# Kernel optimization log

Measured on AMD Instinct MI355X. Metric: run time of the kernel, lower is better.

## Reference

```python
import jax, jax.numpy as jnp
import numpy as np

H = 2048        # hidden size
NK = 16         # key heads
NV = 32         # value heads
DK = 128        # key head dim
DV = 128        # value head dim
K = 4           # conv kernel size
KEY_DIM = NK * DK      # 2048
VAL_DIM = NV * DV      # 4096
CONV_DIM = 2 * KEY_DIM + VAL_DIM  # 8192 (q,k,v pass through the causal conv)
EPS = 1e-6


def setup_inputs() -> dict:
    key = jax.random.key(0)
    ks = jax.random.split(key, 16)
    d = {}
    d["hidden_states"] = jax.random.normal(ks[0], (1, 1, H), jnp.float32)
    for i in range(4):
        d[f"gated_state_{i}"] = 0.1 * jax.random.normal(ks[1 + i], (1, NV, DV, DK), jnp.float32)
        d[f"conv_state_{i}"] = 0.1 * jax.random.normal(ks[5 + i], (1, K - 1, CONV_DIM), jnp.float32)
    # stacked per-layer parameters (leading dim = 4 layers)
    d["W_qkvz"] = 0.02 * jax.random.normal(ks[9], (4, H, 2 * KEY_DIM + 2 * VAL_DIM), jnp.float32)
    d["W_ba"] = 0.02 * jax.random.normal(ks[10], (4, H, 2 * NV), jnp.float32)
    d["conv_w"] = 0.1 * jax.random.normal(ks[11], (4, CONV_DIM, K), jnp.float32)
    d["dt_bias"] = 0.1 * jax.random.normal(ks[12], (4, NV), jnp.float32)
    d["A_log"] = 0.1 * jax.random.normal(ks[13], (4, NV), jnp.float32)
    d["norm_w"] = jnp.ones((4, DV), jnp.float32)
    d["W_out"] = 0.02 * jax.random.normal(ks[14], (4, VAL_DIM, H), jnp.float32)
    return d


def _layer_step(x, S, C, Wq, Wba, cw, dtb, Alog, nw, Wo):
    """One GatedDeltaNet decode step. x:[1,1,H], S:[1,NV,DV,DK], C:[1,K-1,CONV_DIM]."""
    h = x[0, 0]                                  # [H]
    qkvz = h @ Wq                                # [2*KEY + 2*VAL]
    q, k, v, z = jnp.split(qkvz, [KEY_DIM, 2 * KEY_DIM, 2 * KEY_DIM + VAL_DIM])
    ba = h @ Wba
    b, a = ba[:NV], ba[NV:]

    # causal depthwise conv state update + silu
    mixed = jnp.concatenate([q, k, v])           # [CONV_DIM]
    window = jnp.concatenate([C[0], mixed[None]], axis=0)  # [K, CONV_DIM]
    new_C = window[1:][None]                     # [1, K-1, CONV_DIM]
    conv = jax.nn.silu(jnp.einsum('kc,ck->c', window, cw))

    q, k, v = jnp.split(conv, [KEY_DIM, 2 * KEY_DIM])
    q = q.reshape(NK, DK)
    k = k.reshape(NK, DK)
    v = v.reshape(NV, DV)
    # per-head l2 norm on q, k
    q = q * jax.lax.rsqrt(jnp.sum(q * q, -1, keepdims=True) + EPS)
    k = k * jax.lax.rsqrt(jnp.sum(k * k, -1, keepdims=True) + EPS)
    rep = NV // NK
    q = jnp.repeat(q, rep, axis=0)               # [NV, DK]
    k = jnp.repeat(k, rep, axis=0)

    beta = jax.nn.sigmoid(b)                     # [NV]
    g = -jnp.exp(Alog) * jax.nn.softplus(a + dtb)
    decay = jnp.exp(g)                           # [NV]

    # gated delta-rule state update
    S0 = S[0] * decay[:, None, None]             # [NV, DV, DK]
    kv = jnp.einsum('hvd,hd->hv', S0, k)         # [NV, DV]
    S1 = S0 + jnp.einsum('hv,hd->hvd', (v - kv) * beta[:, None], k)
    o = jnp.einsum('hvd,hd->hv', S1, q) * (DK ** -0.5)  # [NV, DV]

    # gated RMSNorm over DV, gated by silu(z)
    zr = z.reshape(NV, DV)
    o = o * jax.lax.rsqrt(jnp.mean(o * o, -1, keepdims=True) + EPS) * nw
    o = o * jax.nn.silu(zr)

    y = (o.reshape(-1) @ Wo)[None, None]         # [1,1,H]
    return y, S1[None], new_C


def _forward(hidden_states, gated_states, conv_states, W_qkvz, W_ba, conv_w, dt_bias, A_log, norm_w, W_out):
    def step(x, inp):
        S, C, Wq, Wba, cw, dtb, Al, nw, Wo = inp
        y, nS, nC = _layer_step(x, S, C, Wq, Wba, cw, dtb, Al, nw, Wo)
        return y, (nS, nC)

    xf, (nS, nC) = jax.lax.scan(
        step, hidden_states,
        (gated_states, conv_states, W_qkvz, W_ba, conv_w, dt_bias, A_log, norm_w, W_out))
    return xf, nS, nC


def reference(hidden_states, gated_state_0, conv_state_0, gated_state_1, conv_state_1,
              gated_state_2, conv_state_2, gated_state_3, conv_state_3,
              W_qkvz, W_ba, conv_w, dt_bias, A_log, norm_w, W_out):
    Ss = jnp.stack([gated_state_0, gated_state_1, gated_state_2, gated_state_3])
    Cs = jnp.stack([conv_state_0, conv_state_1, conv_state_2, conv_state_3])
    xf, nS, nC = _forward(hidden_states, Ss, Cs, W_qkvz, W_ba, conv_w, dt_bias, A_log, norm_w, W_out)
    return (xf, nS[0], nC[0], nS[1], nC[1], nS[2], nC[2], nS[3], nC[3])
```

## Files before the change

kernel.cpp:

```cpp
#include <hip/hip_runtime.h>

#define H_DIM 2048
#define NV 32
#define DK 128
#define DV 128
#define KEY_DIM 2048
#define VAL_DIM 4096
#define CONV_DIM 8192
#define QKVZ_DIM 12288
#define NS_ELEMS (NV * DV * DK)
#define NC_ELEMS (3 * CONV_DIM)
#define NPQ 16
#define NPY 32

typedef float f32x4 __attribute__((ext_vector_type(4)));

__device__ __forceinline__ float silu_f(float x) { return x / (1.f + expf(-x)); }
__device__ __forceinline__ f32x4 ntload4(const float* p) {
  return __builtin_nontemporal_load(reinterpret_cast<const f32x4*>(p));
}

__global__ __launch_bounds__(256) void k_gemv_qkvz(
    const float* __restrict__ hsrc, int hparts,
    const float* __restrict__ Wq, const float* __restrict__ Wba,
    float* __restrict__ qpart, float* __restrict__ bapart)
{
  int bid = blockIdx.x, t = threadIdx.x;
  __shared__ float hs[128];
  __shared__ f32x4 red[256];
  int rb = (bid < 768) ? (bid / 48) * 128 : (bid - 768) * 128;
  if (t < 128) {
    float s = 0.f;
    if (hparts == 1) {
      s = hsrc[rb + t];
    } else {
#pragma unroll
      for (int p = 0; p < NPY; ++p) s += hsrc[p * H_DIM + rb + t];
    }
    hs[t] = s;
  }
  __syncthreads();
  if (bid < 768) {
    int p = bid / 48;
    int cb = (bid % 48) * 256;
    int jj = cb + (t & 63) * 4;
    int i0 = (t >> 6) * 32;
    f32x4 acc = {0.f, 0.f, 0.f, 0.f};
    const float* wp = Wq + (size_t)(rb + i0) * QKVZ_DIM + jj;
#pragma unroll 8
    for (int ii = 0; ii < 32; ++ii) {
      float hv = hs[i0 + ii];
      f32x4 w = ntload4(wp + (size_t)ii * QKVZ_DIM);
      acc += hv * w;
    }
    red[t] = acc;
    __syncthreads();
    if (t < 64) {
      f32x4 o = red[t] + red[t + 64] + red[t + 128] + red[t + 192];
      *reinterpret_cast<f32x4*>(qpart + (size_t)p * QKVZ_DIM + cb + t * 4) = o;
    }
  } else {
    int p = bid - 768;
    int col = t & 63;
    int i0 = (t >> 6) * 32;
    float acc = 0.f;
#pragma unroll 8
    for (int ii = 0; ii < 32; ++ii)
      acc += hs[i0 + ii] * Wba[(size_t)(rb + i0 + ii) * 64 + col];
    red[t].x = acc;
    __syncthreads();
    if (t < 64)
      bapart[p * 64 + t] = red[t].x + red[t + 64].x + red[t + 128].x + red[t + 192].x;
  }
}

__global__ __launch_bounds__(256) void k_state(
    const float* __restrict__ S_in, const float* __restrict__ C_in,
    const float* __restrict__ qpart, const float* __restrict__ bapart,
    const float* __restrict__ conv_w, const float* __restrict__ dt_bias,
    const float* __restrict__ A_log,
    float* __restrict__ nS, float* __restrict__ nC,
    float* __restrict__ o_raw, float* __restrict__ o2part)
{
  int bid = blockIdx.x, t = threadIdx.x;
  if (bid < 128) {
    int hh = bid >> 2, vchunk = bid & 3;
    int kqh = hh >> 1;
    __shared__ float kk[128], qq[128], vv[32], sc[4];
    __shared__ float qs[128], ks[128], vs[32], o2s[8];
    if (t < 128) {
      float s = 0.f;
#pragma unroll
      for (int p = 0; p < NPQ; ++p) s += qpart[(size_t)p * QKVZ_DIM + kqh * 128 + t];
      qs[t] = s;
    } else {
      int u = t - 128;
      float s = 0.f;
#pragma unroll
      for (int p = 0; p < NPQ; ++p) s += qpart[(size_t)p * QKVZ_DIM + KEY_DIM + kqh * 128 + u];
      ks[u] = s;
    }
    if (t < 32) {
      float s = 0.f;
#pragma unroll
      for (int p = 0; p < NPQ; ++p)
        s += qpart[(size_t)p * QKVZ_DIM + 2 * KEY_DIM + hh * 128 + vchunk * 32 + t];
      vs[t] = s;
    }
    float bval = 0.f, aval = 0.f;
    if (t == 160) {
#pragma unroll
      for (int p = 0; p < NPQ; ++p) {
        bval += bapart[p * 64 + hh];
        aval += bapart[p * 64 + 32 + hh];
      }
    }
    __syncthreads();
    auto convval = [&](int c, float last) -> float {
      f32x4 w = *reinterpret_cast<const f32x4*>(conv_w + (size_t)c * 4);
      float val = C_in[c] * w.x + C_in[CONV_DIM + c] * w.y +
                  C_in[2 * CONV_DIM + c] * w.z + last * w.w;
      return silu_f(val);
    };
    if (t < 128) kk[t] = convval(KEY_DIM + kqh * 128 + t, ks[t]);
    else         qq[t - 128] = convval(kqh * 128 + (t - 128), qs[t - 128]);
    __syncthreads();
    if (t < 64) {
      float v = kk[t] * kk[t] + kk[t + 64] * kk[t + 64];
      for (int m = 32; m; m >>= 1) v += __shfl_xor(v, m, 64);
      if (t == 0) sc[0] = v;
    } else if (t < 128) {
      int u = t - 64;
      float v = qq[u] * qq[u] + qq[u + 64] * qq[u + 64];
      for (int m = 32; m; m >>= 1) v += __shfl_xor(v, m, 64);
      if (u == 0) sc[1] = v;
    } else if (t < 160) {
      vv[t - 128] = convval(2 * KEY_DIM + hh * 128 + vchunk * 32 + (t - 128), vs[t - 128]);
    } else if (t == 160) {
      float beta = 1.f / (1.f + expf(-bval));
      float x = aval + dt_bias[hh];
      float sp = (x > 15.f) ? x : log1pf(expf(x));
      sc[2] = beta;
      sc[3] = expf(-expf(A_log[hh]) * sp);
    }
    __syncthreads();
    float rk = rsqrtf(sc[0] + 1e-6f), rq = rsqrtf(sc[1] + 1e-6f);
    float beta = sc[2], decay = sc[3];
    int lane = t & 31;
    int d0 = lane * 4;
    f32x4 k4 = {kk[d0] * rk, kk[d0 + 1] * rk, kk[d0 + 2] * rk, kk[d0 + 3] * rk};
    f32x4 q4 = {qq[d0] * rq, qq[d0 + 1] * rq, qq[d0 + 2] * rq, qq[d0 + 3] * rq};
    float o2loc = 0.f;
    for (int p = 0; p < 4; ++p) {
      int vl = p * 8 + (t >> 5);
      int vrow = vchunk * 32 + vl;
      size_t idx = ((size_t)(hh * 128 + vrow) * 128 + d0);
      f32x4 s = *reinterpret_cast<const f32x4*>(S_in + idx);
      s *= decay;
      float kv = s.x * k4.x + s.y * k4.y + s.z * k4.z + s.w * k4.w;
      for (int m = 16; m; m >>= 1) kv += __shfl_xor(kv, m, 32);
      float dl = (vv[vl] - kv) * beta;
      f32x4 s1 = s + dl * k4;
      *reinterpret_cast<f32x4*>(nS + idx) = s1;
      float op = s1.x * q4.x + s1.y * q4.y + s1.z * q4.z + s1.w * q4.w;
      for (int m = 16; m; m >>= 1) op += __shfl_xor(op, m, 32);
      if (lane == 0) {
        float o = op * 0.088388347648318447f;
        o_raw[hh * 128 + vrow] = o;
        o2loc += o * o;
      }
    }
    if (lane == 0) o2s[t >> 5] = o2loc;
    __syncthreads();
    if (t == 0) {
      float s = 0.f;
#pragma unroll
      for (int w = 0; w < 8; ++w) s += o2s[w];
      o2part[hh * 4 + vchunk] = s;
    }
  } else {
    int gt = (bid - 128) * 256 + t;
    if (gt < NC_ELEMS / 4) {
      int c4 = gt * 4;
      int row = c4 >> 13;
      int cc = c4 & (CONV_DIM - 1);
      f32x4 v;
      if (row < 2) {
        v = *reinterpret_cast<const f32x4*>(C_in + (row + 1) * CONV_DIM + cc);
      } else {
        v = (f32x4){0.f, 0.f, 0.f, 0.f};
#pragma unroll
        for (int p = 0; p < NPQ; ++p)
          v += *reinterpret_cast<const f32x4*>(qpart + (size_t)p * QKVZ_DIM + cc);
      }
      *reinterpret_cast<f32x4*>(nC + row * CONV_DIM + cc) = v;
    }
  }
}

__global__ __launch_bounds__(256) void k_gemv_out(
    const float* __restrict__ o_raw, const float* __restrict__ o2part,
    const float* __restrict__ qpart, const float* __restrict__ norm_w,
    const float* __restrict__ Wo, float* __restrict__ ypart)
{
  int bid = blockIdx.x, t = threadIdx.x;
  int cb = (bid & 7) * 256;
  int hh = bid >> 3;
  int rb = hh * 128;
  __shared__ float of[128];
  __shared__ f32x4 red[256];
  if (t < 128) {
    float o2 = o2part[hh * 4] + o2part[hh * 4 + 1] + o2part[hh * 4 + 2] + o2part[hh * 4 + 3];
    float rs = rsqrtf(o2 * (1.f / 128.f) + 1e-6f);
    float z = 0.f;
#pragma unroll
    for (int p = 0; p < NPQ; ++p) z += qpart[(size_t)p * QKVZ_DIM + CONV_DIM + rb + t];
    of[t] = o_raw[rb + t] * rs * norm_w[t] * silu_f(z);
  }
  __syncthreads();
  int jj = cb + (t & 63) * 4;
  int i0 = (t >> 6) * 32;
  f32x4 acc = {0.f, 0.f, 0.f, 0.f};
  const float* wp = Wo + (size_t)(rb + i0) * H_DIM + jj;
#pragma unroll 8
  for (int ii = 0; ii < 32; ++ii) {
    float ov = of[i0 + ii];
    f32x4 w = ntload4(wp + (size_t)ii * H_DIM);
    acc += ov * w;
  }
  red[t] = acc;
  __syncthreads();
  if (t < 64) {
    f32x4 o = red[t] + red[t + 64] + red[t + 128] + red[t + 192];
    *reinterpret_cast<f32x4*>(ypart + (size_t)hh * H_DIM + cb + t * 4) = o;
  }
}

__global__ __launch_bounds__(256) void k_final(const float* __restrict__ ypart,
                                               float* __restrict__ dst) {
  int c = blockIdx.x * 256 + threadIdx.x;
  float s = 0.f;
#pragma unroll
  for (int p = 0; p < NPY; ++p) s += ypart[p * H_DIM + c];
  dst[c] = s;
}

extern "C" void kernel_launch(void* const* d_in, const int* in_sizes, int n_in,
                              void* d_out, int out_size, void* d_ws, size_t ws_size,
                              hipStream_t stream)
{
  const float* hidden  = (const float*)d_in[0];
  const float* Wq_all  = (const float*)d_in[9];
  const float* Wba_all = (const float*)d_in[10];
  const float* cw_all  = (const float*)d_in[11];
  const float* dtb_all = (const float*)d_in[12];
  const float* Al_all  = (const float*)d_in[13];
  const float* nw_all  = (const float*)d_in[14];
  const float* Wo_all  = (const float*)d_in[15];
  float* out = (float*)d_out;
  float* ws  = (float*)d_ws;

  float* qpart  = ws;
  float* bapart = qpart + NPQ * QKVZ_DIM;
  float* o2part = bapart + NPQ * 64;
  float* ypart  = o2part + 128;
  float* oraw   = ypart + NPY * H_DIM;

  for (int L = 0; L < 4; ++L) {
    const float* hsrc = (L == 0) ? hidden : ypart;
    int hparts        = (L == 0) ? 1 : NPY;
    const float* S_in = (const float*)d_in[1 + 2 * L];
    const float* C_in = (const float*)d_in[2 + 2 * L];
    float* nS = out + 2048 + (size_t)L * (NS_ELEMS + NC_ELEMS);
    float* nC = nS + NS_ELEMS;

    k_gemv_qkvz<<<784, 256, 0, stream>>>(
        hsrc, hparts,
        Wq_all + (size_t)L * H_DIM * QKVZ_DIM,
        Wba_all + (size_t)L * H_DIM * 64,
        qpart, bapart);

    k_state<<<160, 256, 0, stream>>>(
        S_in, C_in, qpart, bapart,
        cw_all + (size_t)L * CONV_DIM * 4, dtb_all + L * 32, Al_all + L * 32,
        nS, nC, oraw, o2part);

    k_gemv_out<<<256, 256, 0, stream>>>(
        oraw, o2part, qpart, nw_all + L * 128,
        Wo_all + (size_t)L * VAL_DIM * H_DIM, ypart);
  }
  k_final<<<8, 256, 0, stream>>>(ypart, out);
}
```

Measured before the change: 141.9 us.

## Fuse state update with output GEMV and retile the QKVZ GEMV

Merges the recurrent-state update and the output projection into one kernel. Each block recomputes a whole head's state update and then does a 128-column slice of the W_out GEMV, with only chunk 0 writing the new state. This removes one launch per layer and the o_raw/o2part round trip, at the cost of each head's state being read and updated redundantly by 16 blocks. The QKVZ GEMV is also retiled into twice as many blocks with 16 rows each, plain loads instead of nontemporal loads, and occupancy hints in launch_bounds.

```diff
diff --git a/kernel.cpp b/kernel.cpp
--- a/kernel.cpp
+++ b/kernel.cpp
@@ -1,26 +1,24 @@
 #include <hip/hip_runtime.h>
 
 #define H_DIM 2048
-#define NV 32
-#define DK 128
-#define DV 128
 #define KEY_DIM 2048
-#define VAL_DIM 4096
 #define CONV_DIM 8192
 #define QKVZ_DIM 12288
-#define NS_ELEMS (NV * DV * DK)
-#define NC_ELEMS (3 * CONV_DIM)
+#define NS_ELEMS 524288
+#define NC_ELEMS 24576
 #define NPQ 16
-#define NPY 32
 
 typedef float f32x4 __attribute__((ext_vector_type(4)));
 
 __device__ __forceinline__ float silu_f(float x) { return x / (1.f + expf(-x)); }
-__device__ __forceinline__ f32x4 ntload4(const float* p) {
-  return __builtin_nontemporal_load(reinterpret_cast<const f32x4*>(p));
-}
-
-__global__ __launch_bounds__(256) void k_gemv_qkvz(
+__device__ __forceinline__ f32x4 ld4(const float* p) {
+  return *reinterpret_cast<const f32x4*>(p);
+}
+__device__ __forceinline__ void st4(float* p, f32x4 v) {
+  *reinterpret_cast<f32x4*>(p) = v;
+}
+
+__global__ __launch_bounds__(256, 6) void k_qkvz(
     const float* __restrict__ hsrc, int hparts,
     const float* __restrict__ Wq, const float* __restrict__ Wba,
     float* __restrict__ qpart, float* __restrict__ bapart)
@@ -28,102 +26,87 @@
   int bid = blockIdx.x, t = threadIdx.x;
   __shared__ float hs[128];
   __shared__ f32x4 red[256];
-  int rb = (bid < 768) ? (bid / 48) * 128 : (bid - 768) * 128;
+  int rb = (bid < 1536) ? (bid / 96) * 128 : (bid - 1536) * 128;
   if (t < 128) {
     float s = 0.f;
     if (hparts == 1) {
       s = hsrc[rb + t];
     } else {
 #pragma unroll
-      for (int p = 0; p < NPY; ++p) s += hsrc[p * H_DIM + rb + t];
+      for (int p = 0; p < 32; ++p) s += hsrc[p * H_DIM + rb + t];
     }
     hs[t] = s;
   }
   __syncthreads();
-  if (bid < 768) {
-    int p = bid / 48;
-    int cb = (bid % 48) * 256;
-    int jj = cb + (t & 63) * 4;
-    int i0 = (t >> 6) * 32;
+  if (bid < 1536) {
+    int p = bid / 96, chunk = bid % 96;
+    int rg = t >> 5, cg = t & 31;
+    const float* wp = Wq + (size_t)(rb + rg * 16) * QKVZ_DIM + chunk * 128 + cg * 4;
     f32x4 acc = {0.f, 0.f, 0.f, 0.f};
-    const float* wp = Wq + (size_t)(rb + i0) * QKVZ_DIM + jj;
-#pragma unroll 8
-    for (int ii = 0; ii < 32; ++ii) {
-      float hv = hs[i0 + ii];
-      f32x4 w = ntload4(wp + (size_t)ii * QKVZ_DIM);
-      acc += hv * w;
-    }
+#pragma unroll
+    for (int ii = 0; ii < 16; ++ii)
+      acc += hs[rg * 16 + ii] * ld4(wp + (size_t)ii * QKVZ_DIM);
     red[t] = acc;
     __syncthreads();
-    if (t < 64) {
-      f32x4 o = red[t] + red[t + 64] + red[t + 128] + red[t + 192];
-      *reinterpret_cast<f32x4*>(qpart + (size_t)p * QKVZ_DIM + cb + t * 4) = o;
+    if (t < 32) {
+      f32x4 o = red[t] + red[t + 32] + red[t + 64] + red[t + 96] +
+                red[t + 128] + red[t + 160] + red[t + 192] + red[t + 224];
+      st4(qpart + (size_t)p * QKVZ_DIM + chunk * 128 + t * 4, o);
     }
   } else {
-    int p = bid - 768;
-    int col = t & 63;
-    int i0 = (t >> 6) * 32;
-    float acc = 0.f;
-#pragma unroll 8
+    int r = bid - 1536;
+    int col = t & 63, rowg = t >> 6;
+    float a = 0.f;
+#pragma unroll
     for (int ii = 0; ii < 32; ++ii)
-      acc += hs[i0 + ii] * Wba[(size_t)(rb + i0 + ii) * 64 + col];
-    red[t].x = acc;
+      a += hs[rowg * 32 + ii] * Wba[(size_t)(rb + rowg * 32 + ii) * 64 + col];
+    red[t].x = a;
     __syncthreads();
     if (t < 64)
-      bapart[p * 64 + t] = red[t].x + red[t + 64].x + red[t + 128].x + red[t + 192].x;
-  }
-}
-
-__global__ __launch_bounds__(256) void k_state(
+      bapart[r * 64 + t] = red[t].x + red[t + 64].x + red[t + 128].x + red[t + 192].x;
+  }
+}
+
+__global__ __launch_bounds__(256, 4) void k_stateout(
     const float* __restrict__ S_in, const float* __restrict__ C_in,
     const float* __restrict__ qpart, const float* __restrict__ bapart,
-    const float* __restrict__ conv_w, const float* __restrict__ dt_bias,
-    const float* __restrict__ A_log,
-    float* __restrict__ nS, float* __restrict__ nC,
-    float* __restrict__ o_raw, float* __restrict__ o2part)
+    const float* __restrict__ cw, const float* __restrict__ dtb,
+    const float* __restrict__ Al, const float* __restrict__ nw,
+    const float* __restrict__ Wo,
+    float* __restrict__ nS, float* __restrict__ nC, float* __restrict__ ypart)
 {
   int bid = blockIdx.x, t = threadIdx.x;
-  if (bid < 128) {
-    int hh = bid >> 2, vchunk = bid & 3;
-    int kqh = hh >> 1;
-    __shared__ float kk[128], qq[128], vv[32], sc[4];
-    __shared__ float qs[128], ks[128], vs[32], o2s[8];
-    if (t < 128) {
+  if (bid < 512) {
+    int hh = bid >> 4, chunk = bid & 15, kqh = hh >> 1;
+    __shared__ float kk[128], qq[128], vvf[128], zz[128], of[128], sc[8];
+    auto red16 = [&](int c) -> float {
       float s = 0.f;
 #pragma unroll
-      for (int p = 0; p < NPQ; ++p) s += qpart[(size_t)p * QKVZ_DIM + kqh * 128 + t];
-      qs[t] = s;
-    } else {
-      int u = t - 128;
-      float s = 0.f;
-#pragma unroll
-      for (int p = 0; p < NPQ; ++p) s += qpart[(size_t)p * QKVZ_DIM + KEY_DIM + kqh * 128 + u];
-      ks[u] = s;
-    }
-    if (t < 32) {
-      float s = 0.f;
-#pragma unroll
-      for (int p = 0; p < NPQ; ++p)
-        s += qpart[(size_t)p * QKVZ_DIM + 2 * KEY_DIM + hh * 128 + vchunk * 32 + t];
-      vs[t] = s;
-    }
-    float bval = 0.f, aval = 0.f;
-    if (t == 160) {
-#pragma unroll
-      for (int p = 0; p < NPQ; ++p) {
-        bval += bapart[p * 64 + hh];
-        aval += bapart[p * 64 + 32 + hh];
-      }
-    }
-    __syncthreads();
+      for (int p = 0; p < NPQ; ++p) s += qpart[(size_t)p * QKVZ_DIM + c];
+      return s;
+    };
     auto convval = [&](int c, float last) -> float {
-      f32x4 w = *reinterpret_cast<const f32x4*>(conv_w + (size_t)c * 4);
+      f32x4 w = ld4(cw + (size_t)c * 4);
       float val = C_in[c] * w.x + C_in[CONV_DIM + c] * w.y +
                   C_in[2 * CONV_DIM + c] * w.z + last * w.w;
       return silu_f(val);
     };
-    if (t < 128) kk[t] = convval(KEY_DIM + kqh * 128 + t, ks[t]);
-    else         qq[t - 128] = convval(kqh * 128 + (t - 128), qs[t - 128]);
+    if (t < 128) {
+      int c = KEY_DIM + kqh * 128 + t;
+      kk[t] = convval(c, red16(c));
+    } else {
+      int u = t - 128;
+      int c = kqh * 128 + u;
+      qq[u] = convval(c, red16(c));
+    }
+    __syncthreads();
+    if (t < 128) {
+      int c = 2 * KEY_DIM + hh * 128 + t;
+      vvf[t] = convval(c, red16(c));
+    } else {
+      int u = t - 128;
+      zz[u] = red16(CONV_DIM + hh * 128 + u);
+    }
     __syncthreads();
     if (t < 64) {
       float v = kk[t] * kk[t] + kk[t + 64] * kk[t + 64];
@@ -134,105 +117,88 @@
       float v = qq[u] * qq[u] + qq[u + 64] * qq[u + 64];
       for (int m = 32; m; m >>= 1) v += __shfl_xor(v, m, 64);
       if (u == 0) sc[1] = v;
-    } else if (t < 160) {
-      vv[t - 128] = convval(2 * KEY_DIM + hh * 128 + vchunk * 32 + (t - 128), vs[t - 128]);
-    } else if (t == 160) {
-      float beta = 1.f / (1.f + expf(-bval));
-      float x = aval + dt_bias[hh];
+    } else if (t == 128) {
+      float bs = 0.f;
+#pragma unroll
+      for (int p = 0; p < NPQ; ++p) bs += bapart[p * 64 + hh];
+      sc[2] = 1.f / (1.f + expf(-bs));
+    } else if (t == 129) {
+      float as = 0.f;
+#pragma unroll
+      for (int p = 0; p < NPQ; ++p) as += bapart[p * 64 + 32 + hh];
+      float x = as + dtb[hh];
       float sp = (x > 15.f) ? x : log1pf(expf(x));
-      sc[2] = beta;
-      sc[3] = expf(-expf(A_log[hh]) * sp);
-    }
-    __syncthreads();
-    float rk = rsqrtf(sc[0] + 1e-6f), rq = rsqrtf(sc[1] + 1e-6f);
-    float beta = sc[2], decay = sc[3];
-    int lane = t & 31;
-    int d0 = lane * 4;
-    f32x4 k4 = {kk[d0] * rk, kk[d0 + 1] * rk, kk[d0 + 2] * rk, kk[d0 + 3] * rk};
-    f32x4 q4 = {qq[d0] * rq, qq[d0 + 1] * rq, qq[d0 + 2] * rq, qq[d0 + 3] * rq};
-    float o2loc = 0.f;
-    for (int p = 0; p < 4; ++p) {
-      int vl = p * 8 + (t >> 5);
-      int vrow = vchunk * 32 + vl;
-      size_t idx = ((size_t)(hh * 128 + vrow) * 128 + d0);
-      f32x4 s = *reinterpret_cast<const f32x4*>(S_in + idx);
-      s *= decay;
-      float kv = s.x * k4.x + s.y * k4.y + s.z * k4.z + s.w * k4.w;
-      for (int m = 16; m; m >>= 1) kv += __shfl_xor(kv, m, 32);
-      float dl = (vv[vl] - kv) * beta;
-      f32x4 s1 = s + dl * k4;
-      *reinterpret_cast<f32x4*>(nS + idx) = s1;
-      float op = s1.x * q4.x + s1.y * q4.y + s1.z * q4.z + s1.w * q4.w;
-      for (int m = 16; m; m >>= 1) op += __shfl_xor(op, m, 32);
-      if (lane == 0) {
-        float o = op * 0.088388347648318447f;
-        o_raw[hh * 128 + vrow] = o;
-        o2loc += o * o;
+      sc[3] = expf(-expf(Al[hh]) * sp);
+    }
+    __syncthreads();
+    {
+      float rk = rsqrtf(sc[0] + 1e-6f), rq = rsqrtf(sc[1] + 1e-6f);
+      float beta = sc[2], decay = sc[3];
+      int grp = t >> 5, lane = t & 31;
+      int d0 = lane * 4;
+      f32x4 k4 = {kk[d0] * rk, kk[d0 + 1] * rk, kk[d0 + 2] * rk, kk[d0 + 3] * rk};
+      f32x4 q4 = {qq[d0] * rq, qq[d0 + 1] * rq, qq[d0 + 2] * rq, qq[d0 + 3] * rq};
+#pragma unroll 4
+      for (int j = 0; j < 16; ++j) {
+        int row = j * 8 + grp;
+        size_t idx = ((size_t)(hh * 128 + row)) * 128 + d0;
+        f32x4 s = ld4(S_in + idx);
+        s *= decay;
+        float kv = s.x * k4.x + s.y * k4.y + s.z * k4.z + s.w * k4.w;
+        for (int m = 16; m; m >>= 1) kv += __shfl_xor(kv, m, 32);
+        float dl = (vvf[row] - kv) * beta;
+        f32x4 s1 = s + dl * k4;
+        if (chunk == 0) st4(nS + idx, s1);
+        float op = s1.x * q4.x + s1.y * q4.y + s1.z * q4.z + s1.w * q4.w;
+        for (int m = 16; m; m >>= 1) op += __shfl_xor(op, m, 32);
+        if (lane == 0) of[row] = op * 0.088388347648318447f;
       }
     }
-    if (lane == 0) o2s[t >> 5] = o2loc;
-    __syncthreads();
-    if (t == 0) {
-      float s = 0.f;
-#pragma unroll
-      for (int w = 0; w < 8; ++w) s += o2s[w];
-      o2part[hh * 4 + vchunk] = s;
+    __syncthreads();
+    if (t < 64) {
+      float v = of[t] * of[t] + of[t + 64] * of[t + 64];
+      for (int m = 32; m; m >>= 1) v += __shfl_xor(v, m, 64);
+      if (t == 0) sc[4] = v;
+    }
+    __syncthreads();
+    if (t < 128) {
+      float rs = rsqrtf(sc[4] * (1.f / 128.f) + 1e-6f);
+      of[t] = of[t] * rs * nw[t] * silu_f(zz[t]);
+    }
+    __syncthreads();
+    {
+      __shared__ f32x4 red[256];
+      int rg = t >> 5, cg = t & 31;
+      const float* wp = Wo + (size_t)(hh * 128 + rg * 16) * H_DIM + chunk * 128 + cg * 4;
+      f32x4 acc = {0.f, 0.f, 0.f, 0.f};
+#pragma unroll
+      for (int ii = 0; ii < 16; ++ii)
+        acc += of[rg * 16 + ii] * ld4(wp + (size_t)ii * H_DIM);
+      red[t] = acc;
+      __syncthreads();
+      if (t < 32) {
+        f32x4 o = red[t] + red[t + 32] + red[t + 64] + red[t + 96] +
+                  red[t + 128] + red[t + 160] + red[t + 192] + red[t + 224];
+        st4(ypart + (size_t)hh * H_DIM + chunk * 128 + t * 4, o);
+      }
     }
   } else {
-    int gt = (bid - 128) * 256 + t;
+    int gt = (bid - 512) * 256 + t;
     if (gt < NC_ELEMS / 4) {
       int c4 = gt * 4;
       int row = c4 >> 13;
       int cc = c4 & (CONV_DIM - 1);
       f32x4 v;
       if (row < 2) {
-        v = *reinterpret_cast<const f32x4*>(C_in + (row + 1) * CONV_DIM + cc);
+        v = ld4(C_in + (row + 1) * CONV_DIM + cc);
       } else {
         v = (f32x4){0.f, 0.f, 0.f, 0.f};
 #pragma unroll
         for (int p = 0; p < NPQ; ++p)
-          v += *reinterpret_cast<const f32x4*>(qpart + (size_t)p * QKVZ_DIM + cc);
+          v += ld4(qpart + (size_t)p * QKVZ_DIM + cc);
       }
-      *reinterpret_cast<f32x4*>(nC + row * CONV_DIM + cc) = v;
-    }
-  }
-}
-
-__global__ __launch_bounds__(256) void k_gemv_out(
-    const float* __restrict__ o_raw, const float* __restrict__ o2part,
-    const float* __restrict__ qpart, const float* __restrict__ norm_w,
-    const float* __restrict__ Wo, float* __restrict__ ypart)
-{
-  int bid = blockIdx.x, t = threadIdx.x;
-  int cb = (bid & 7) * 256;
-  int hh = bid >> 3;
-  int rb = hh * 128;
-  __shared__ float of[128];
-  __shared__ f32x4 red[256];
-  if (t < 128) {
-    float o2 = o2part[hh * 4] + o2part[hh * 4 + 1] + o2part[hh * 4 + 2] + o2part[hh * 4 + 3];
-    float rs = rsqrtf(o2 * (1.f / 128.f) + 1e-6f);
-    float z = 0.f;
-#pragma unroll
-    for (int p = 0; p < NPQ; ++p) z += qpart[(size_t)p * QKVZ_DIM + CONV_DIM + rb + t];
-    of[t] = o_raw[rb + t] * rs * norm_w[t] * silu_f(z);
-  }
-  __syncthreads();
-  int jj = cb + (t & 63) * 4;
-  int i0 = (t >> 6) * 32;
-  f32x4 acc = {0.f, 0.f, 0.f, 0.f};
-  const float* wp = Wo + (size_t)(rb + i0) * H_DIM + jj;
-#pragma unroll 8
-  for (int ii = 0; ii < 32; ++ii) {
-    float ov = of[i0 + ii];
-    f32x4 w = ntload4(wp + (size_t)ii * H_DIM);
-    acc += ov * w;
-  }
-  red[t] = acc;
-  __syncthreads();
-  if (t < 64) {
-    f32x4 o = red[t] + red[t + 64] + red[t + 128] + red[t + 192];
-    *reinterpret_cast<f32x4*>(ypart + (size_t)hh * H_DIM + cb + t * 4) = o;
+      st4(nC + row * CONV_DIM + cc, v);
+    }
   }
 }
 
@@ -241,7 +207,7 @@
   int c = blockIdx.x * 256 + threadIdx.x;
   float s = 0.f;
 #pragma unroll
-  for (int p = 0; p < NPY; ++p) s += ypart[p * H_DIM + c];
+  for (int p = 0; p < 32; ++p) s += ypart[p * H_DIM + c];
   dst[c] = s;
 }
 
@@ -258,36 +224,32 @@
   const float* nw_all  = (const float*)d_in[14];
   const float* Wo_all  = (const float*)d_in[15];
   float* out = (float*)d_out;
-  float* ws  = (float*)d_ws;
-
-  float* qpart  = ws;
-  float* bapart = qpart + NPQ * QKVZ_DIM;
-  float* o2part = bapart + NPQ * 64;
-  float* ypart  = o2part + 128;
-  float* oraw   = ypart + NPY * H_DIM;
+  float* f   = (float*)d_ws;
+
+  float* qpart  = f;  f += NPQ * QKVZ_DIM;
+  float* bapart = f;  f += NPQ * 64;
+  float* ypart  = f;  f += 32 * H_DIM;
 
   for (int L = 0; L < 4; ++L) {
     const float* hsrc = (L == 0) ? hidden : ypart;
-    int hparts        = (L == 0) ? 1 : NPY;
+    int hparts        = (L == 0) ? 1 : 32;
     const float* S_in = (const float*)d_in[1 + 2 * L];
     const float* C_in = (const float*)d_in[2 + 2 * L];
     float* nS = out + 2048 + (size_t)L * (NS_ELEMS + NC_ELEMS);
     float* nC = nS + NS_ELEMS;
 
-    k_gemv_qkvz<<<784, 256, 0, stream>>>(
+    k_qkvz<<<1552, 256, 0, stream>>>(
         hsrc, hparts,
         Wq_all + (size_t)L * H_DIM * QKVZ_DIM,
         Wba_all + (size_t)L * H_DIM * 64,
         qpart, bapart);
 
-    k_state<<<160, 256, 0, stream>>>(
+    k_stateout<<<536, 256, 0, stream>>>(
         S_in, C_in, qpart, bapart,
-        cw_all + (size_t)L * CONV_DIM * 4, dtb_all + L * 32, Al_all + L * 32,
-        nS, nC, oraw, o2part);
-
-    k_gemv_out<<<256, 256, 0, stream>>>(
-        oraw, o2part, qpart, nw_all + L * 128,
-        Wo_all + (size_t)L * VAL_DIM * H_DIM, ypart);
+        cw_all + (size_t)L * CONV_DIM * 4,
+        dtb_all + L * 32, Al_all + L * 32, nw_all + L * 128,
+        Wo_all + (size_t)L * 4096 * H_DIM,
+        nS, nC, ypart);
   }
   k_final<<<8, 256, 0, stream>>>(ypart, out);
 }
```

New measurement: 186.4 us. 31.3% more time.
